# Kernel tuning notes

Hardware: AMD Instinct MI355X
Metric: run time of the kernel (lower is better)

## Reference

```python
import jax, jax.numpy as jnp
import numpy as np

ALPHA = 16.0
RANK = 64
SCALING = ALPHA / RANK


def setup_inputs() -> dict:
    key = jax.random.key(0)
    k1, k2, k3, k4, k5 = jax.random.split(key, 5)
    B, S, DIN, DOUT = 4, 4096, 4096, 4096
    x = jax.random.normal(k1, (B, S, DIN), dtype=jnp.float32)
    lora_A = jax.random.normal(k2, (RANK, DIN), dtype=jnp.float32) / np.sqrt(DIN)
    lora_B = jax.random.normal(k3, (DOUT, RANK), dtype=jnp.float32)
    lora_A_scale = jax.random.uniform(k4, (RANK,), dtype=jnp.float32, minval=0.5, maxval=1.5)
    lora_B_scale = jax.random.uniform(k5, (DOUT,), dtype=jnp.float32, minval=0.5, maxval=1.5)
    return {"x": x, "lora_A": lora_A, "lora_B": lora_B,
            "lora_A_scale": lora_A_scale, "lora_B_scale": lora_B_scale}


def reference(x, lora_A, lora_B, lora_A_scale, lora_B_scale):
    # INT8 dequant path: quantized.float() * scale.unsqueeze(-1)
    A_dq = lora_A * lora_A_scale[:, None]          # [rank, in]
    B_dq = lora_B * lora_B_scale[:, None]          # [out, rank]
    # x @ A.T -> [B, S, rank]; then @ B.T -> [B, S, out]; final scaling
    h = jnp.einsum('bsi,ri->bsr', x, A_dq)
    out = jnp.einsum('bsr,or->bso', h, B_dq)
    return out * SCALING
```

## Files before the change

### kernel.cpp

```cpp
#include <hip/hip_runtime.h>


#define M_TOTAL 16384
#define DIN     4096
#define DOUT    4096
#define RANK    64

typedef __bf16 bf16_8 __attribute__((ext_vector_type(8)));
typedef __bf16 bf16_4 __attribute__((ext_vector_type(4)));
typedef float  f32x4  __attribute__((ext_vector_type(4)));

__global__ __launch_bounds__(256) void prep_kernel(
    const float* __restrict__ A, const float* __restrict__ Bm,
    const float* __restrict__ sA, const float* __restrict__ sB,
    __bf16* __restrict__ Abf, __bf16* __restrict__ Bbf) {
  int i = (blockIdx.x * 256 + threadIdx.x) * 4;
  float4 a = *(const float4*)(A + i);
  float sa = sA[i >> 12];
  bf16_4 va;
  va[0] = (__bf16)(a.x * sa); va[1] = (__bf16)(a.y * sa);
  va[2] = (__bf16)(a.z * sa); va[3] = (__bf16)(a.w * sa);
  *(bf16_4*)(Abf + i) = va;

  float4 b = *(const float4*)(Bm + i);
  float sb = sB[i >> 6] * 0.25f;
  bf16_4 vb;
  vb[0] = (__bf16)(b.x * sb); vb[1] = (__bf16)(b.y * sb);
  vb[2] = (__bf16)(b.z * sb); vb[3] = (__bf16)(b.w * sb);
  *(bf16_4*)(Bbf + i) = vb;
}

__global__ __launch_bounds__(256, 2) void gemm1_kernel(
    const float* __restrict__ x, const __bf16* __restrict__ Abf,
    __bf16* __restrict__ h) {
  __shared__ __bf16 xs[32 * 72];
  __shared__ __bf16 as[64 * 72];

  const int t = threadIdx.x;
  const int mBase = blockIdx.x * 32;

  const int xrow = t >> 3;
  const int xc   = t & 7;
  const float* xg = x + (size_t)(mBase + xrow) * DIN + xc * 4;

  const int arow = t >> 2;
  const int ac   = t & 3;
  const __bf16* ag = Abf + (size_t)arow * DIN + ac * 8;

  const int lane = t & 63;
  const int w    = t >> 6;
  const int mt   = w >> 1;
  const int nh   = w & 1;
  const int lr   = lane & 15;
  const int quad = lane >> 4;

  f32x4 acc0 = {0.f, 0.f, 0.f, 0.f};
  f32x4 acc1 = {0.f, 0.f, 0.f, 0.f};

  float4 f0 = *(const float4*)(xg);
  float4 f1 = *(const float4*)(xg + 32);
  bf16_8 a0 = *(const bf16_8*)(ag);
  bf16_8 a1 = *(const bf16_8*)(ag + 32);

  for (int k0 = 0; k0 < DIN; k0 += 64) {
    __syncthreads();

    bf16_4 v;
    v[0] = (__bf16)f0.x; v[1] = (__bf16)f0.y;
    v[2] = (__bf16)f0.z; v[3] = (__bf16)f0.w;
    *(bf16_4*)&xs[xrow * 72 + xc * 4] = v;
    v[0] = (__bf16)f1.x; v[1] = (__bf16)f1.y;
    v[2] = (__bf16)f1.z; v[3] = (__bf16)f1.w;
    *(bf16_4*)&xs[xrow * 72 + xc * 4 + 32] = v;
    *(bf16_8*)&as[arow * 72 + ac * 8] = a0;
    *(bf16_8*)&as[arow * 72 + ac * 8 + 32] = a1;

    __syncthreads();

    if (k0 + 64 < DIN) {
      f0 = *(const float4*)(xg + (k0 + 64));
      f1 = *(const float4*)(xg + (k0 + 64) + 32);
      a0 = *(const bf16_8*)(ag + (k0 + 64));
      a1 = *(const bf16_8*)(ag + (k0 + 64) + 32);
    }

#pragma unroll
    for (int ks = 0; ks < 2; ++ks) {
      bf16_8 af  = *(const bf16_8*)&xs[(mt * 16 + lr) * 72 + ks * 32 + quad * 8];
      bf16_8 bf0 = *(const bf16_8*)&as[(nh * 32 + lr) * 72 + ks * 32 + quad * 8];
      bf16_8 bf1 = *(const bf16_8*)&as[(nh * 32 + 16 + lr) * 72 + ks * 32 + quad * 8];
      acc0 = __builtin_amdgcn_mfma_f32_16x16x32_bf16(af, bf0, acc0, 0, 0, 0);
      acc1 = __builtin_amdgcn_mfma_f32_16x16x32_bf16(af, bf1, acc1, 0, 0, 0);
    }
  }

  const int m = mBase + mt * 16 + quad * 4;
  const int n = nh * 32 + lr;
#pragma unroll
  for (int i = 0; i < 4; ++i) {
    h[(size_t)(m + i) * RANK + n]      = (__bf16)acc0[i];
    h[(size_t)(m + i) * RANK + n + 16] = (__bf16)acc1[i];
  }
}

__global__ __launch_bounds__(256, 4) void gemm2_kernel(
    const __bf16* __restrict__ h, const __bf16* __restrict__ Bbf,
    float* __restrict__ out) {
  __shared__ __bf16 hs[128 * 72];
  __shared__ __bf16 bs[128 * 72];

  const int t = threadIdx.x;
  const int mBase = blockIdx.y * 128;
  const int nBase = blockIdx.x * 128;

  {
    const __bf16* hg = h   + (size_t)mBase * RANK;
    const __bf16* bg = Bbf + (size_t)nBase * RANK;
#pragma unroll
    for (int l = 0; l < 4; ++l) {
      int q = l * 2048 + t * 8;
      bf16_8 hv = *(const bf16_8*)(hg + q);
      bf16_8 bv = *(const bf16_8*)(bg + q);
      int row = q >> 6;
      int col = q & 63;
      *(bf16_8*)&hs[row * 72 + col] = hv;
      *(bf16_8*)&bs[row * 72 + col] = bv;
    }
  }
  __syncthreads();

  const int lane = t & 63;
  const int w    = t >> 6;
  const int wm   = w >> 1;
  const int wn   = w & 1;
  const int lr   = lane & 15;
  const int quad = lane >> 4;

  f32x4 acc[4][4];
#pragma unroll
  for (int mt = 0; mt < 4; ++mt)
#pragma unroll
    for (int nt = 0; nt < 4; ++nt)
      acc[mt][nt] = (f32x4){0.f, 0.f, 0.f, 0.f};

#pragma unroll
  for (int ks = 0; ks < 2; ++ks) {
    bf16_8 af[4], bfr[4];
#pragma unroll
    for (int mt = 0; mt < 4; ++mt)
      af[mt] = *(const bf16_8*)&hs[(wm * 64 + mt * 16 + lr) * 72 + ks * 32 + quad * 8];
#pragma unroll
    for (int nt = 0; nt < 4; ++nt)
      bfr[nt] = *(const bf16_8*)&bs[(wn * 64 + nt * 16 + lr) * 72 + ks * 32 + quad * 8];
#pragma unroll
    for (int mt = 0; mt < 4; ++mt)
#pragma unroll
      for (int nt = 0; nt < 4; ++nt)
        acc[mt][nt] = __builtin_amdgcn_mfma_f32_16x16x32_bf16(af[mt], bfr[nt], acc[mt][nt], 0, 0, 0);
  }

#pragma unroll
  for (int mt = 0; mt < 4; ++mt) {
    int m = mBase + wm * 64 + mt * 16 + quad * 4;
#pragma unroll
    for (int nt = 0; nt < 4; ++nt) {
      int n = nBase + wn * 64 + nt * 16 + lr;
#pragma unroll
      for (int i = 0; i < 4; ++i)
        out[(size_t)(m + i) * DOUT + n] = acc[mt][nt][i];
    }
  }
}

extern "C" void kernel_launch(void* const* d_in, const int* in_sizes, int n_in,
                              void* d_out, int out_size, void* d_ws, size_t ws_size,
                              hipStream_t stream) {
  const float* x  = (const float*)d_in[0];
  const float* A  = (const float*)d_in[1];
  const float* Bm = (const float*)d_in[2];
  const float* sA = (const float*)d_in[3];
  const float* sB = (const float*)d_in[4];
  float* out = (float*)d_out;

  __bf16* Abf = (__bf16*)d_ws;
  __bf16* Bbf = Abf + (size_t)RANK * DIN;
  __bf16* h   = Bbf + (size_t)DOUT * RANK;

  prep_kernel<<<256, 256, 0, stream>>>(A, Bm, sA, sB, Abf, Bbf);
  gemm1_kernel<<<M_TOTAL / 32, 256, 0, stream>>>(x, Abf, h);
  gemm2_kernel<<<dim3(DOUT / 128, M_TOTAL / 128), 256, 0, stream>>>(h, Bbf, out);
}
```

Before: 476.2 us.

## Fuse both LoRA GEMMs into one single-wave kernel with register prefetch

Replaces the separate x@A and h@B kernels with one kernel where each 64-thread wave computes a 16-row h tile directly from global memory using register double-buffering, stages it through a tiny LDS buffer, then streams the full output row block using B fragments loaded from global memory. This removes the intermediate h round-trip, one launch, and the LDS staging of x and A. It risks low occupancy and latency exposure, since only 1024 single-wave blocks exist and A and B are re-read per wave through cache.

```diff
diff --git a/kernel.cpp b/kernel.cpp
--- a/kernel.cpp
+++ b/kernel.cpp
@@ -30,145 +30,104 @@
   *(bf16_4*)(Bbf + i) = vb;
 }
 
-__global__ __launch_bounds__(256, 2) void gemm1_kernel(
+#define LOAD_CHUNK(XV, AV, K0)                                                 \
+  {                                                                            \
+    XV[0] = *(const float4*)(xg + (K0));                                       \
+    XV[1] = *(const float4*)(xg + (K0) + 4);                                   \
+    XV[2] = *(const float4*)(xg + (K0) + 32);                                  \
+    XV[3] = *(const float4*)(xg + (K0) + 36);                                  \
+    _Pragma("unroll") for (int nt = 0; nt < 4; ++nt) {                         \
+      AV[nt]     = *(const bf16_8*)(agl + nt * 16 * DIN + (K0));               \
+      AV[4 + nt] = *(const bf16_8*)(agl + nt * 16 * DIN + (K0) + 32);          \
+    }                                                                          \
+  }
+
+#define COMPUTE_CHUNK(XV, AV)                                                  \
+  {                                                                            \
+    _Pragma("unroll") for (int kc = 0; kc < 2; ++kc) {                         \
+      float4 u = XV[kc * 2], v = XV[kc * 2 + 1];                               \
+      bf16_8 af;                                                               \
+      af[0] = (__bf16)u.x; af[1] = (__bf16)u.y;                                \
+      af[2] = (__bf16)u.z; af[3] = (__bf16)u.w;                                \
+      af[4] = (__bf16)v.x; af[5] = (__bf16)v.y;                                \
+      af[6] = (__bf16)v.z; af[7] = (__bf16)v.w;                                \
+      _Pragma("unroll") for (int nt = 0; nt < 4; ++nt)                         \
+        hacc[nt] = __builtin_amdgcn_mfma_f32_16x16x32_bf16(                    \
+            af, AV[kc * 4 + nt], hacc[nt], 0, 0, 0);                           \
+    }                                                                          \
+  }
+
+#define LOAD_B(BV, NC)                                                         \
+  {                                                                            \
+    _Pragma("unroll") for (int nt = 0; nt < 4; ++nt) {                         \
+      BV[nt * 2]     = *(const bf16_8*)(bg + ((NC) + nt * 16) * RANK);         \
+      BV[nt * 2 + 1] = *(const bf16_8*)(bg + ((NC) + nt * 16) * RANK + 32);    \
+    }                                                                          \
+  }
+
+#define COMPUTE_STORE(BV, NC)                                                  \
+  {                                                                            \
+    f32x4 acc[4];                                                              \
+    _Pragma("unroll") for (int nt = 0; nt < 4; ++nt)                           \
+        acc[nt] = (f32x4){0.f, 0.f, 0.f, 0.f};                                 \
+    _Pragma("unroll") for (int nt = 0; nt < 4; ++nt) {                         \
+      acc[nt] = __builtin_amdgcn_mfma_f32_16x16x32_bf16(                       \
+          hf0, BV[nt * 2], acc[nt], 0, 0, 0);                                  \
+      acc[nt] = __builtin_amdgcn_mfma_f32_16x16x32_bf16(                       \
+          hf1, BV[nt * 2 + 1], acc[nt], 0, 0, 0);                              \
+    }                                                                          \
+    _Pragma("unroll") for (int nt = 0; nt < 4; ++nt)                           \
+      _Pragma("unroll") for (int i = 0; i < 4; ++i)                            \
+        og[(size_t)i * DOUT + (NC) + nt * 16] = acc[nt][i];                    \
+  }
+
+__global__ __launch_bounds__(64) void fused_kernel(
     const float* __restrict__ x, const __bf16* __restrict__ Abf,
-    __bf16* __restrict__ h) {
-  __shared__ __bf16 xs[32 * 72];
-  __shared__ __bf16 as[64 * 72];
+    const __bf16* __restrict__ Bbf, float* __restrict__ out) {
+  __shared__ __bf16 hs[16 * 80];
 
-  const int t = threadIdx.x;
-  const int mBase = blockIdx.x * 32;
-
-  const int xrow = t >> 3;
-  const int xc   = t & 7;
-  const float* xg = x + (size_t)(mBase + xrow) * DIN + xc * 4;
-
-  const int arow = t >> 2;
-  const int ac   = t & 3;
-  const __bf16* ag = Abf + (size_t)arow * DIN + ac * 8;
-
-  const int lane = t & 63;
-  const int w    = t >> 6;
-  const int mt   = w >> 1;
-  const int nh   = w & 1;
+  const int lane = threadIdx.x;
   const int lr   = lane & 15;
   const int quad = lane >> 4;
+  const int mBase = blockIdx.x * 16;
 
-  f32x4 acc0 = {0.f, 0.f, 0.f, 0.f};
-  f32x4 acc1 = {0.f, 0.f, 0.f, 0.f};
+  const float*  xg  = x   + (size_t)(mBase + lr) * DIN + quad * 8;
+  const __bf16* agl = Abf + (size_t)lr * DIN + quad * 8;
 
-  float4 f0 = *(const float4*)(xg);
-  float4 f1 = *(const float4*)(xg + 32);
-  bf16_8 a0 = *(const bf16_8*)(ag);
-  bf16_8 a1 = *(const bf16_8*)(ag + 32);
+  f32x4 hacc[4];
+#pragma unroll
+  for (int nt = 0; nt < 4; ++nt) hacc[nt] = (f32x4){0.f, 0.f, 0.f, 0.f};
 
-  for (int k0 = 0; k0 < DIN; k0 += 64) {
-    __syncthreads();
-
-    bf16_4 v;
-    v[0] = (__bf16)f0.x; v[1] = (__bf16)f0.y;
-    v[2] = (__bf16)f0.z; v[3] = (__bf16)f0.w;
-    *(bf16_4*)&xs[xrow * 72 + xc * 4] = v;
-    v[0] = (__bf16)f1.x; v[1] = (__bf16)f1.y;
-    v[2] = (__bf16)f1.z; v[3] = (__bf16)f1.w;
-    *(bf16_4*)&xs[xrow * 72 + xc * 4 + 32] = v;
-    *(bf16_8*)&as[arow * 72 + ac * 8] = a0;
-    *(bf16_8*)&as[arow * 72 + ac * 8 + 32] = a1;
-
-    __syncthreads();
-
-    if (k0 + 64 < DIN) {
-      f0 = *(const float4*)(xg + (k0 + 64));
-      f1 = *(const float4*)(xg + (k0 + 64) + 32);
-      a0 = *(const bf16_8*)(ag + (k0 + 64));
-      a1 = *(const bf16_8*)(ag + (k0 + 64) + 32);
-    }
-
-#pragma unroll
-    for (int ks = 0; ks < 2; ++ks) {
-      bf16_8 af  = *(const bf16_8*)&xs[(mt * 16 + lr) * 72 + ks * 32 + quad * 8];
-      bf16_8 bf0 = *(const bf16_8*)&as[(nh * 32 + lr) * 72 + ks * 32 + quad * 8];
-      bf16_8 bf1 = *(const bf16_8*)&as[(nh * 32 + 16 + lr) * 72 + ks * 32 + quad * 8];
-      acc0 = __builtin_amdgcn_mfma_f32_16x16x32_bf16(af, bf0, acc0, 0, 0, 0);
-      acc1 = __builtin_amdgcn_mfma_f32_16x16x32_bf16(af, bf1, acc1, 0, 0, 0);
-    }
-  }
-
-  const int m = mBase + mt * 16 + quad * 4;
-  const int n = nh * 32 + lr;
-#pragma unroll
-  for (int i = 0; i < 4; ++i) {
-    h[(size_t)(m + i) * RANK + n]      = (__bf16)acc0[i];
-    h[(size_t)(m + i) * RANK + n + 16] = (__bf16)acc1[i];
-  }
-}
-
-__global__ __launch_bounds__(256, 4) void gemm2_kernel(
-    const __bf16* __restrict__ h, const __bf16* __restrict__ Bbf,
-    float* __restrict__ out) {
-  __shared__ __bf16 hs[128 * 72];
-  __shared__ __bf16 bs[128 * 72];
-
-  const int t = threadIdx.x;
-  const int mBase = blockIdx.y * 128;
-  const int nBase = blockIdx.x * 128;
-
-  {
-    const __bf16* hg = h   + (size_t)mBase * RANK;
-    const __bf16* bg = Bbf + (size_t)nBase * RANK;
-#pragma unroll
-    for (int l = 0; l < 4; ++l) {
-      int q = l * 2048 + t * 8;
-      bf16_8 hv = *(const bf16_8*)(hg + q);
-      bf16_8 bv = *(const bf16_8*)(bg + q);
-      int row = q >> 6;
-      int col = q & 63;
-      *(bf16_8*)&hs[row * 72 + col] = hv;
-      *(bf16_8*)&bs[row * 72 + col] = bv;
-    }
-  }
-  __syncthreads();
-
-  const int lane = t & 63;
-  const int w    = t >> 6;
-  const int wm   = w >> 1;
-  const int wn   = w & 1;
-  const int lr   = lane & 15;
-  const int quad = lane >> 4;
-
-  f32x4 acc[4][4];
-#pragma unroll
-  for (int mt = 0; mt < 4; ++mt)
-#pragma unroll
-    for (int nt = 0; nt < 4; ++nt)
-      acc[mt][nt] = (f32x4){0.f, 0.f, 0.f, 0.f};
-
-#pragma unroll
-  for (int ks = 0; ks < 2; ++ks) {
-    bf16_8 af[4], bfr[4];
-#pragma unroll
-    for (int mt = 0; mt < 4; ++mt)
-      af[mt] = *(const bf16_8*)&hs[(wm * 64 + mt * 16 + lr) * 72 + ks * 32 + quad * 8];
-#pragma unroll
-    for (int nt = 0; nt < 4; ++nt)
-      bfr[nt] = *(const bf16_8*)&bs[(wn * 64 + nt * 16 + lr) * 72 + ks * 32 + quad * 8];
-#pragma unroll
-    for (int mt = 0; mt < 4; ++mt)
-#pragma unroll
-      for (int nt = 0; nt < 4; ++nt)
-        acc[mt][nt] = __builtin_amdgcn_mfma_f32_16x16x32_bf16(af[mt], bfr[nt], acc[mt][nt], 0, 0, 0);
+  float4 xva[4], xvb[4];
+  bf16_8 ava[8], avb[8];
+  LOAD_CHUNK(xva, ava, 0);
+  LOAD_CHUNK(xvb, avb, 64);
+  for (int k0 = 0; k0 < DIN; k0 += 128) {
+    COMPUTE_CHUNK(xva, ava);
+    if (k0 + 128 < DIN) LOAD_CHUNK(xva, ava, k0 + 128);
+    COMPUTE_CHUNK(xvb, avb);
+    if (k0 + 192 < DIN) LOAD_CHUNK(xvb, avb, k0 + 192);
   }
 
 #pragma unroll
-  for (int mt = 0; mt < 4; ++mt) {
-    int m = mBase + wm * 64 + mt * 16 + quad * 4;
+  for (int nt = 0; nt < 4; ++nt)
 #pragma unroll
-    for (int nt = 0; nt < 4; ++nt) {
-      int n = nBase + wn * 64 + nt * 16 + lr;
-#pragma unroll
-      for (int i = 0; i < 4; ++i)
-        out[(size_t)(m + i) * DOUT + n] = acc[mt][nt][i];
-    }
+    for (int i = 0; i < 4; ++i)
+      hs[(quad * 4 + i) * 80 + nt * 16 + lr] = (__bf16)hacc[nt][i];
+  __syncthreads();
+  const bf16_8 hf0 = *(const bf16_8*)&hs[lr * 80 + quad * 8];
+  const bf16_8 hf1 = *(const bf16_8*)&hs[lr * 80 + 32 + quad * 8];
+
+  const __bf16* bg = Bbf + (size_t)lr * RANK + quad * 8;
+  float*        og = out + (size_t)(mBase + quad * 4) * DOUT + lr;
+
+  bf16_8 bva[8], bvb[8];
+  LOAD_B(bva, 0);
+  for (int nc = 0; nc < DOUT; nc += 128) {
+    LOAD_B(bvb, nc + 64);
+    COMPUTE_STORE(bva, nc);
+    if (nc + 128 < DOUT) LOAD_B(bva, nc + 128);
+    COMPUTE_STORE(bvb, nc + 64);
   }
 }
 
@@ -184,9 +143,7 @@
 
   __bf16* Abf = (__bf16*)d_ws;
   __bf16* Bbf = Abf + (size_t)RANK * DIN;
-  __bf16* h   = Bbf + (size_t)DOUT * RANK;
 
   prep_kernel<<<256, 256, 0, stream>>>(A, Bm, sA, sB, Abf, Bbf);
-  gemm1_kernel<<<M_TOTAL / 32, 256, 0, stream>>>(x, Abf, h);
-  gemm2_kernel<<<dim3(DOUT / 128, M_TOTAL / 128), 256, 0, stream>>>(h, Bbf, out);
+  fused_kernel<<<M_TOTAL / 16, 64, 0, stream>>>(x, Abf, Bbf, out);
 }
```

Result: slower. 528.6 us (+11.0%).
